# Kernel optimization log

Measured on AMD Instinct MI355X. Metric: run time of the kernel, lower is better.

The kernel has to match this reference:

```python
import jax, jax.numpy as jnp
import numpy as np

N_USERS = 100000
N_ITEMS = 50000
N_NODES = N_USERS + N_ITEMS
NNZ = 4000000
DIM = 64
N_LAYERS = 3
BATCH = 4096


def setup_inputs() -> dict:
    key = jax.random.key(0)
    k = jax.random.split(key, 7)
    users = jax.random.randint(k[0], (BATCH,), 0, N_USERS, dtype=jnp.int32)
    items = jax.random.randint(k[1], (BATCH,), 0, N_ITEMS, dtype=jnp.int32)
    edge_src = jax.random.randint(k[2], (NNZ,), 0, N_NODES, dtype=jnp.int32)
    edge_dst = jax.random.randint(k[3], (NNZ,), 0, N_NODES, dtype=jnp.int32)
    # normalized adjacency values (positive weights, like D^-1/2 A D^-1/2)
    edge_val = jax.random.uniform(k[4], (NNZ,), dtype=jnp.float32)
    user_emb = 0.1 * jax.random.normal(k[5], (N_USERS, DIM), dtype=jnp.float32)
    item_emb = 0.1 * jax.random.normal(k[6], (N_ITEMS, DIM), dtype=jnp.float32)
    return {"users": users, "items": items, "edge_src": edge_src,
            "edge_dst": edge_dst, "edge_val": edge_val,
            "user_emb": user_emb, "item_emb": item_emb}


def _spmm(edge_src, edge_dst, edge_val, emb):
    # y[dst] += val * emb[src]  (sparse adjacency @ dense embedding)
    vals = edge_val[:, None] * emb[edge_src]          # [nnz, d]
    return jax.ops.segment_sum(vals, edge_dst, num_segments=N_NODES)


def reference(users, items, edge_src, edge_dst, edge_val, user_emb, item_emb):
    all_emb = jnp.concatenate([user_emb, item_emb], axis=0)  # [N, d]
    acc = all_emb
    x = all_emb
    for _ in range(N_LAYERS):
        x = _spmm(edge_src, edge_dst, edge_val, x)
        acc = acc + x
    light_out = acc / jnp.asarray(N_LAYERS + 1, dtype=acc.dtype)  # layer mean
    all_users = light_out[:N_USERS]
    all_items = light_out[N_USERS:]
    u = all_users[users]                              # [B, d]
    i = all_items[items]                              # [B, d]
    scores = jnp.sum(u * i, axis=-1)                  # [B]
    return jax.nn.sigmoid(scores)
```

## Files before the change

### kernel.cpp

```cpp
#include <hip/hip_runtime.h>
#include <hip/hip_fp16.h>

#define N_USERS 100000
#define N_ITEMS 50000
#define N_NODES 150000
#define DIM 64
#define NNZ 4000000
#define BATCH 4096

#define NBUCK 586
#define CAP   7680
#define NB_C  256
#define CHUNK (NNZ / NB_C)

typedef __half f16;

__device__ __forceinline__ float h2f(f16 h) { return __half2float(h); }

__global__ void initt_k(int* __restrict__ gticket) {
    int i = blockIdx.x * blockDim.x + threadIdx.x;
    if (i < NBUCK) gticket[i] = i * CAP;
}

__global__ __launch_bounds__(512) void coarse_k(
        const int* __restrict__ src, const int* __restrict__ dst,
        const float* __restrict__ val, int* __restrict__ gticket,
        int2* __restrict__ ev) {
    __shared__ int hist[NBUCK];
    __shared__ int base[NBUCK];
    __shared__ int tick[NBUCK];
    int t  = threadIdx.x;
    int lo = blockIdx.x * CHUNK;
    int hi = lo + CHUNK;
    for (int i = t; i < NBUCK; i += blockDim.x) hist[i] = 0;
    __syncthreads();
    for (int e = lo + t; e < hi; e += blockDim.x)
        atomicAdd(&hist[dst[e] >> 8], 1);
    __syncthreads();
    for (int i = t; i < NBUCK; i += blockDim.x) {
        base[i] = atomicAdd(&gticket[i], hist[i]);
        tick[i] = 0;
    }
    __syncthreads();
    for (int e = lo + t; e < hi; e += blockDim.x) {
        int d  = dst[e];
        int bk = d >> 8;
        int p  = base[bk] + atomicAdd(&tick[bk], 1);
        ev[p]  = make_int2(src[e] | ((d & 255) << 18), __float_as_int(val[e]));
    }
}

__global__ void scanC_k(const int* __restrict__ gticket, int* __restrict__ bktbase) {
    __shared__ int sh[1024];
    int tid = threadIdx.x;
    int v = (tid < NBUCK) ? (gticket[tid] - tid * CAP) : 0;
    sh[tid] = v;
    __syncthreads();
    for (int off = 1; off < 1024; off <<= 1) {
        int t = (tid >= off) ? sh[tid - off] : 0;
        __syncthreads();
        sh[tid] += t;
        __syncthreads();
    }
    if (tid < NBUCK) bktbase[tid] = sh[tid] - v;
}

__global__ void fine_k(const int* __restrict__ gticket, const int* __restrict__ bktbase,
                       const int2* __restrict__ ev,
                       int2* __restrict__ sorted, int* __restrict__ row) {
    __shared__ int hist[256];
    __shared__ int sh[256];
    int k = blockIdx.x, t = threadIdx.x;
    hist[t] = 0;
    __syncthreads();
    int cnt = gticket[k] - k * CAP;
    int s0  = k * CAP;
    for (int i = t; i < cnt; i += 256)
        atomicAdd(&hist[(ev[s0 + i].x >> 18) & 255], 1);
    __syncthreads();
    int v = hist[t];
    sh[t] = v;
    __syncthreads();
    for (int off = 1; off < 256; off <<= 1) {
        int tmp = (t >= off) ? sh[t - off] : 0;
        __syncthreads();
        sh[t] += tmp;
        __syncthreads();
    }
    int excl    = sh[t] - v;
    int rowbase = bktbase[k];
    int node    = (k << 8) + t;
    if (node < N_NODES) row[node] = rowbase + excl;
    if (k == 0 && t == 0) row[N_NODES] = NNZ;
    hist[t] = excl;
    __syncthreads();
    for (int i = t; i < cnt; i += 256) {
        int2 r = ev[s0 + i];
        int p  = atomicAdd(&hist[(r.x >> 18) & 255], 1);
        sorted[rowbase + p] = make_int2(r.x & 0x3FFFF, r.y);
    }
}

__global__ void conv_k(const float4* __restrict__ ue, const float4* __restrict__ ie,
                       ushort4* __restrict__ X0) {
    int i = blockIdx.x * blockDim.x + threadIdx.x;
    const int total  = N_NODES * DIM / 4;
    const int ubound = N_USERS * DIM / 4;
    if (i >= total) return;
    float4 v = (i < ubound) ? ue[i] : ie[i - ubound];
    f16 a = __float2half(v.x), b = __float2half(v.y);
    f16 c = __float2half(v.z), d = __float2half(v.w);
    ushort4 o;
    o.x = *reinterpret_cast<ushort*>(&a);
    o.y = *reinterpret_cast<ushort*>(&b);
    o.z = *reinterpret_cast<ushort*>(&c);
    o.w = *reinterpret_cast<ushort*>(&d);
    X0[i] = o;
}

__global__ void gather16_k(const int* __restrict__ row, const int2* __restrict__ se,
                           const uint2* __restrict__ X4, uint2* __restrict__ Y4) {
    int wid  = (blockIdx.x * blockDim.x + threadIdx.x) >> 6;
    int lane = threadIdx.x & 63;
    if (wid >= N_NODES) return;
    int sub  = lane >> 4;
    int quad = lane & 15;
    int beg = row[wid], end = row[wid + 1];
    float a0 = 0.f, a1 = 0.f, a2 = 0.f, a3 = 0.f;
    for (int base = beg; base < end; base += 64) {
        int rem = end - base;
        int n = rem < 64 ? rem : 64;
        int2 evv = make_int2(0, 0);
        if (lane < n) evv = se[base + lane];
        int ng = (n + 3) >> 2;
        for (int g0 = 0; g0 < ng; g0 += 4) {
            uint2 xr[4]; float vs[4];
            #pragma unroll
            for (int k = 0; k < 4; ++k) {
                int ei = ((g0 + k) << 2) + sub;
                int sx = __shfl(evv.x, ei, 64);
                vs[k]  = __int_as_float(__shfl(evv.y, ei, 64));
                xr[k]  = X4[((size_t)sx << 4) + quad];
            }
            #pragma unroll
            for (int k = 0; k < 4; ++k) {
                float2 f0 = __half22float2(*reinterpret_cast<const half2*>(&xr[k].x));
                float2 f1 = __half22float2(*reinterpret_cast<const half2*>(&xr[k].y));
                a0 += vs[k] * f0.x;
                a1 += vs[k] * f0.y;
                a2 += vs[k] * f1.x;
                a3 += vs[k] * f1.y;
            }
        }
    }
    a0 += __shfl_xor(a0, 16, 64);  a1 += __shfl_xor(a1, 16, 64);
    a2 += __shfl_xor(a2, 16, 64);  a3 += __shfl_xor(a3, 16, 64);
    a0 += __shfl_xor(a0, 32, 64);  a1 += __shfl_xor(a1, 32, 64);
    a2 += __shfl_xor(a2, 32, 64);  a3 += __shfl_xor(a3, 32, 64);
    if (sub == 0) {
        half2 h0 = __floats2half2_rn(a0, a1);
        half2 h1 = __floats2half2_rn(a2, a3);
        uint2 o;
        o.x = *reinterpret_cast<uint*>(&h0);
        o.y = *reinterpret_cast<uint*>(&h1);
        Y4[((size_t)wid << 4) + quad] = o;
    }
}

__global__ void gather3_k(const int* __restrict__ users, const int* __restrict__ items,
                          const int* __restrict__ row, const int2* __restrict__ se,
                          const f16* __restrict__ X, f16* __restrict__ X3p) {
    int s    = (blockIdx.x * blockDim.x + threadIdx.x) >> 6;
    int lane = threadIdx.x & 63;
    if (s >= 2 * BATCH) return;
    int wid = (s < BATCH) ? users[s] : (N_USERS + items[s - BATCH]);
    int beg = row[wid], end = row[wid + 1];
    float acc = 0.f;
    for (int base = beg; base < end; base += 64) {
        int rem = end - base;
        int n = rem < 64 ? rem : 64;
        int2 evv = make_int2(0, 0);
        if (lane < n) evv = se[base + lane];
        int n8 = (n + 7) & ~7;
        for (int j = 0; j < n8; j += 8) {
            float xv[8], vv[8];
            #pragma unroll
            for (int k = 0; k < 8; ++k) {
                int sr = __shfl(evv.x, j + k, 64);
                vv[k] = __int_as_float(__shfl(evv.y, j + k, 64));
                xv[k] = h2f(X[(sr << 6) + lane]);
            }
            #pragma unroll
            for (int k = 0; k < 8; ++k) acc += vv[k] * xv[k];
        }
    }
    X3p[(s << 6) + lane] = __float2half(acc);
}

__global__ void final_k(const int* __restrict__ users, const int* __restrict__ items,
                        const float* __restrict__ ue, const float* __restrict__ ie,
                        const f16* __restrict__ X1, const f16* __restrict__ X2,
                        const f16* __restrict__ X3p, float* __restrict__ out) {
    int b    = blockIdx.x * (blockDim.x / 64) + (threadIdx.x / 64);
    int lane = threadIdx.x & 63;
    if (b >= BATCH) return;
    int u  = users[b];
    int it = items[b];
    int uo = (u << 6) + lane;
    int io = ((N_USERS + it) << 6) + lane;
    float au = ue[uo]               + h2f(X1[uo]) + h2f(X2[uo]) + h2f(X3p[(b << 6) + lane]);
    float ai = ie[(it << 6) + lane] + h2f(X1[io]) + h2f(X2[io]) + h2f(X3p[((b + BATCH) << 6) + lane]);
    float p = au * ai * (1.0f / 16.0f);
    #pragma unroll
    for (int off = 32; off; off >>= 1) p += __shfl_down(p, off, 64);
    if (lane == 0) out[b] = 1.0f / (1.0f + __expf(-p));
}

extern "C" void kernel_launch(void* const* d_in, const int* in_sizes, int n_in,
                              void* d_out, int out_size, void* d_ws, size_t ws_size,
                              hipStream_t stream) {
    const int*   users = (const int*)  d_in[0];
    const int*   items = (const int*)  d_in[1];
    const int*   esrc  = (const int*)  d_in[2];
    const int*   edst  = (const int*)  d_in[3];
    const float* eval  = (const float*)d_in[4];
    const float* uemb  = (const float*)d_in[5];
    const float* iemb  = (const float*)d_in[6];
    float*       out   = (float*)      d_out;

    const size_t XB = (size_t)N_NODES * DIM * sizeof(f16);
    char* ws = (char*)d_ws;
    f16*  X0     = (f16*) (ws);
    f16*  X1     = (f16*) (ws + XB);
    f16*  X2     = (f16*) (ws + 2 * XB);
    f16*  X3p    = (f16*) (ws + 3 * XB);
    int2* sorted = (int2*)(ws + 3 * XB + ((size_t)2 * BATCH * DIM * 2 + 255 & ~255UL));
    char* p      = (char*)sorted + (size_t)NNZ * sizeof(int2);
    int*  row     = (int*)(p);                 p += ((size_t)(N_NODES + 1) * 4 + 255) & ~255UL;
    int*  gticket = (int*)(p);                 p += (NBUCK * 4 + 255) & ~255UL;
    int*  bktbase = (int*)(p);
    int2* cev = (int2*)(ws);

    initt_k<<<(NBUCK + 255) / 256, 256, 0, stream>>>(gticket);
    coarse_k<<<NB_C, 512, 0, stream>>>(esrc, edst, eval, gticket, cev);
    scanC_k<<<1, 1024, 0, stream>>>(gticket, bktbase);
    fine_k<<<NBUCK, 256, 0, stream>>>(gticket, bktbase, cev, sorted, row);

    conv_k<<<(N_NODES * DIM / 4 + 255) / 256, 256, 0, stream>>>(
        (const float4*)uemb, (const float4*)iemb, (ushort4*)X0);

    const int gthreads = N_NODES * 64;
    gather16_k<<<(gthreads + 255) / 256, 256, 0, stream>>>(row, sorted,
                                                           (const uint2*)X0, (uint2*)X1);
    gather16_k<<<(gthreads + 255) / 256, 256, 0, stream>>>(row, sorted,
                                                           (const uint2*)X1, (uint2*)X2);
    gather3_k<<<(2 * BATCH * 64 + 255) / 256, 256, 0, stream>>>(users, items, row,
                                                                sorted, X2, X3p);

    final_k<<<(BATCH * 64 + 255) / 256, 256, 0, stream>>>(users, items, uemb, iemb,
                                                          X1, X2, X3p, out);
}
```

Before: 247.1 us.

## Stage coarse bucket scatter in LDS and write buckets contiguously

The coarse bucketing kernel now scatters each block's edges into a shared-memory buffer ordered by bucket, using a wave-level prefix scan of the local histogram. It then copies each bucket's run to global memory as contiguous writes instead of random 8-byte global scatters. Block size also doubles to 1024 threads. The kernel needs about 125 KB of dynamic LDS, which limits occupancy to one block per CU and relies on the larger LDS on this hardware.

```diff
diff --git a/kernel.cpp b/kernel.cpp
--- a/kernel.cpp
+++ b/kernel.cpp
@@ -22,31 +22,57 @@
     if (i < NBUCK) gticket[i] = i * CAP;
 }
 
-__global__ __launch_bounds__(512) void coarse_k(
+__global__ __launch_bounds__(1024) void coarse_k(
         const int* __restrict__ src, const int* __restrict__ dst,
         const float* __restrict__ val, int* __restrict__ gticket,
         int2* __restrict__ ev) {
-    __shared__ int hist[NBUCK];
-    __shared__ int base[NBUCK];
-    __shared__ int tick[NBUCK];
-    int t  = threadIdx.x;
-    int lo = blockIdx.x * CHUNK;
-    int hi = lo + CHUNK;
-    for (int i = t; i < NBUCK; i += blockDim.x) hist[i] = 0;
-    __syncthreads();
-    for (int e = lo + t; e < hi; e += blockDim.x)
+    extern __shared__ char smem[];
+    int2* buf   = (int2*)smem;
+    int*  hist  = (int*)(smem + (size_t)CHUNK * 8);
+    int*  lbase = hist  + NBUCK;
+    int*  gbase = lbase + NBUCK;
+    int*  tick  = gbase + NBUCK;
+    const int t  = threadIdx.x;
+    const int nt = blockDim.x;
+    const int lo = blockIdx.x * CHUNK;
+    const int hi = lo + CHUNK;
+
+    for (int i = t; i < NBUCK; i += nt) { hist[i] = 0; tick[i] = 0; }
+    __syncthreads();
+    for (int e = lo + t; e < hi; e += nt)
         atomicAdd(&hist[dst[e] >> 8], 1);
     __syncthreads();
-    for (int i = t; i < NBUCK; i += blockDim.x) {
-        base[i] = atomicAdd(&gticket[i], hist[i]);
-        tick[i] = 0;
-    }
-    __syncthreads();
-    for (int e = lo + t; e < hi; e += blockDim.x) {
+    if (t < 64) {
+        int lane = t;
+        int carry = 0;
+        for (int c = 0; c < (NBUCK + 63) / 64; ++c) {
+            int idx = c * 64 + lane;
+            int v = (idx < NBUCK) ? hist[idx] : 0;
+            int s = v;
+            #pragma unroll
+            for (int off = 1; off < 64; off <<= 1) {
+                int u = __shfl_up(s, off, 64);
+                if (lane >= off) s += u;
+            }
+            if (idx < NBUCK) lbase[idx] = carry + s - v;
+            carry += __shfl(s, 63, 64);
+        }
+    }
+    for (int i = t; i < NBUCK; i += nt)
+        gbase[i] = atomicAdd(&gticket[i], hist[i]);
+    __syncthreads();
+    for (int e = lo + t; e < hi; e += nt) {
         int d  = dst[e];
         int bk = d >> 8;
-        int p  = base[bk] + atomicAdd(&tick[bk], 1);
-        ev[p]  = make_int2(src[e] | ((d & 255) << 18), __float_as_int(val[e]));
+        int p  = lbase[bk] + atomicAdd(&tick[bk], 1);
+        buf[p] = make_int2(src[e] | ((d & 255) << 18), __float_as_int(val[e]));
+    }
+    __syncthreads();
+    int wid = t >> 6, lane = t & 63, nw = nt >> 6;
+    for (int bk = wid; bk < NBUCK; bk += nw) {
+        int cnt = hist[bk], lb = lbase[bk], gb = gbase[bk];
+        for (int i = lane; i < cnt; i += 64)
+            ev[gb + i] = buf[lb + i];
     }
 }
 
@@ -241,8 +267,12 @@
     int*  bktbase = (int*)(p);
     int2* cev = (int2*)(ws);
 
+    const size_t CLDS = (size_t)CHUNK * 8 + (size_t)4 * NBUCK * 4;
+    hipFuncSetAttribute((const void*)coarse_k,
+                        hipFuncAttributeMaxDynamicSharedMemorySize, (int)CLDS);
+
     initt_k<<<(NBUCK + 255) / 256, 256, 0, stream>>>(gticket);
-    coarse_k<<<NB_C, 512, 0, stream>>>(esrc, edst, eval, gticket, cev);
+    coarse_k<<<NB_C, 1024, CLDS, stream>>>(esrc, edst, eval, gticket, cev);
     scanC_k<<<1, 1024, 0, stream>>>(gticket, bktbase);
     fine_k<<<NBUCK, 256, 0, stream>>>(gticket, bktbase, cev, sorted, row);
 
```

After: 234.0 us. -5.3%, faster.
